# Kernel optimization log

Measured on AMD Instinct MI355X. Metric: run time of the kernel, lower is better.

Reference implementation:

```python
import jax, jax.numpy as jnp
import numpy as np

B, I, J, K, F = 16, 2048, 1024, 1024, 32

def _xavier(key, shape):
    fan_in, fan_out = shape[0], shape[1]
    limit = np.sqrt(6.0 / (fan_in + fan_out))
    return jax.random.uniform(key, shape, jnp.float32, -limit, limit)

def setup_inputs() -> dict:
    key = jax.random.key(0)
    kx, kwx, kwy, kwz = jax.random.split(key, 4)
    return {
        "matrix_batch": jax.random.normal(kx, (B, I, J), jnp.float32),
        "W_x": _xavier(kwx, (I, F)),
        "W_y": _xavier(kwy, (J, F)),
        "W_z": _xavier(kwz, (K, F)),
    }

def reference(matrix_batch, W_x, W_y, W_z):
    # Original math: W[i,j,k] = sum_f Wx[i,f]*Wy[j,f]*Wz[k,f];
    #                out[b,i,k] = sum_j x[b,i,j] * W[i,j,k]
    # Fused two-stage contraction (never materializes the (I,J,K) core):
    # t[b,i,f] = (sum_j x[b,i,j] Wy[j,f]) * Wx[i,f]
    t = jnp.einsum('bij,jf->bif', matrix_batch, W_y) * W_x[None, :, :]
    out = jnp.einsum('bif,kf->bik', t, W_z)  # (B, I, K)
    return out
```

## Files before the change

### kernel.cpp

```cpp
#include <hip/hip_runtime.h>
#include <hip/hip_bf16.h>
#include <string.h>

constexpr int kI = 2048;
constexpr int kJ = 1024;
constexpr int kK = 1024;
constexpr int kF = 32;
constexpr int kRows = 16 * 2048;

typedef __attribute__((ext_vector_type(8))) short short8v;
typedef __attribute__((ext_vector_type(4))) float f32x4;

__device__ inline unsigned short bf16_hi_bits(float v) {
    __hip_bfloat16 h = __float2bfloat16(v);
    unsigned short s;
    memcpy(&s, &h, 2);
    return s;
}
__device__ inline float bf16_bits_to_f(unsigned short s) {
    unsigned u = (unsigned)s << 16;
    float f;
    memcpy(&f, &u, 4);
    return f;
}
__device__ inline short8v as_s8(uint4 u) {
    union { uint4 a; short8v b; } c;
    c.a = u;
    return c.b;
}
__device__ inline void gl_lds16(const void* g, void* l) {
    __builtin_amdgcn_global_load_lds(
        (const __attribute__((address_space(1))) void*)g,
        (__attribute__((address_space(3))) void*)l,
        16, 0, 0);
}

__global__ __launch_bounds__(128)
void ge_prepack(const float* __restrict__ Wy, uint4* __restrict__ wyp)
{
    const int e  = blockIdx.x * 128 + threadIdx.x;
    const int l  = e & 63;
    const int h  = (e >> 6) & 1;
    const int tf = (e >> 7) & 1;
    const int ks = e >> 8;
    const int f  = (l & 15) + tf * 16;
    const int j0 = ks * 32 + (l >> 4) * 8;

    unsigned d[4];
#pragma unroll
    for (int p = 0; p < 4; ++p) {
        const float v0 = Wy[(size_t)(j0 + 2 * p) * kF + f];
        const float v1 = Wy[(size_t)(j0 + 2 * p + 1) * kF + f];
        unsigned short s0, s1;
        if (h == 0) {
            s0 = bf16_hi_bits(v0);
            s1 = bf16_hi_bits(v1);
        } else {
            s0 = bf16_hi_bits(v0 - bf16_bits_to_f(bf16_hi_bits(v0)));
            s1 = bf16_hi_bits(v1 - bf16_bits_to_f(bf16_hi_bits(v1)));
        }
        d[p] = (unsigned)s0 | ((unsigned)s1 << 16);
    }
    wyp[e] = make_uint4(d[0], d[1], d[2], d[3]);
}

__global__ __launch_bounds__(128)
void ge_prepack_z(const float* __restrict__ Wz, uint4* __restrict__ wzp)
{
    const int e  = blockIdx.x * 128 + threadIdx.x;
    const int l  = e & 63;
    const int h  = (e >> 6) & 1;
    const int nt = e >> 7;
    const int n  = nt * 16 + (l & 15);
    const int f0 = (l >> 4) * 8;

    unsigned d[4];
#pragma unroll
    for (int p = 0; p < 4; ++p) {
        const float v0 = Wz[(size_t)n * kF + f0 + 2 * p];
        const float v1 = Wz[(size_t)n * kF + f0 + 2 * p + 1];
        unsigned short s0, s1;
        if (h == 0) {
            s0 = bf16_hi_bits(v0);
            s1 = bf16_hi_bits(v1);
        } else {
            s0 = bf16_hi_bits(v0 - bf16_bits_to_f(bf16_hi_bits(v0)));
            s1 = bf16_hi_bits(v1 - bf16_bits_to_f(bf16_hi_bits(v1)));
        }
        d[p] = (unsigned)s0 | ((unsigned)s1 << 16);
    }
    wzp[e] = make_uint4(d[0], d[1], d[2], d[3]);
}

__global__ __launch_bounds__(256, 2)
void ge_fused_mfma(const float* __restrict__ x,
                   const float* __restrict__ Wx,
                   const uint4* __restrict__ wyp,
                   const uint4* __restrict__ wzp,
                   float* __restrict__ out)
{
    __shared__ __align__(16) char smem[73728];
    float4* xb4 = reinterpret_cast<float4*>(smem);
    uint4*  bb4 = reinterpret_cast<uint4*>(smem + 49152);
    uint4*  zb  = reinterpret_cast<uint4*>(smem);
    float*  t2  = reinterpret_cast<float*>(smem + 49152);

    const int tid  = threadIdx.x;
    const int lane = tid & 63;
    const int wv   = tid >> 6;
    const int mrow = lane & 15;
    const int g    = lane >> 4;
    const int rowBase = blockIdx.x * 64;

    f32x4 c0 = {0.f, 0.f, 0.f, 0.f};
    f32x4 c1 = {0.f, 0.f, 0.f, 0.f};

#define STAGE(buf, ti)                                                  \
    {                                                                   \
        _Pragma("unroll")                                               \
        for (int q = 0; q < 4; ++q) {                                   \
            const int srow = wv * 16 + q * 4 + (lane >> 4);             \
            const int sc   = lane & 15;                                 \
            gl_lds16(x + (size_t)(rowBase + srow) * kJ + (ti) * 64      \
                       + 4 * (sc ^ (srow & 7)),                         \
                     &xb4[(buf) * 1024 + (wv * 16 + q * 4) * 16]);      \
        }                                                               \
        _Pragma("unroll")                                               \
        for (int q = 0; q < 2; ++q)                                     \
            gl_lds16(wyp + (size_t)(ti) * 512 + wv * 128 + q * 64 + lane, \
                     &bb4[(buf) * 512 + wv * 128 + q * 64]);            \
    }

    STAGE(0, 0)

#pragma unroll
    for (int ti = 0; ti < 16; ++ti) {
        const int bufR = ti % 3;
        if (ti < 15) {
            STAGE((ti + 1) % 3, ti + 1)
            asm volatile("s_waitcnt vmcnt(6) lgkmcnt(0)" ::: "memory");
        } else {
            asm volatile("s_waitcnt vmcnt(0) lgkmcnt(0)" ::: "memory");
        }
        asm volatile("s_barrier" ::: "memory");
        __builtin_amdgcn_sched_barrier(0);

#pragma unroll
        for (int kk2 = 0; kk2 < 2; ++kk2) {
            const uint4 b0h = bb4[bufR * 512 + kk2 * 256 + lane];
            const uint4 b0l = bb4[bufR * 512 + kk2 * 256 + 64 + lane];
            const uint4 b1h = bb4[bufR * 512 + kk2 * 256 + 128 + lane];
            const uint4 b1l = bb4[bufR * 512 + kk2 * 256 + 192 + lane];

            const int s0 = (kk2 * 8 + g * 2) ^ (mrow & 7);
            const int s1 = (kk2 * 8 + g * 2 + 1) ^ (mrow & 7);
            const float4 xa = xb4[bufR * 1024 + (wv * 16 + mrow) * 16 + s0];
            const float4 xc = xb4[bufR * 1024 + (wv * 16 + mrow) * 16 + s1];
            const float xv[8] = {xa.x, xa.y, xa.z, xa.w,
                                 xc.x, xc.y, xc.z, xc.w};

            short8v ah, al;
#pragma unroll
            for (int e = 0; e < 8; ++e) {
                const unsigned short hb = bf16_hi_bits(xv[e]);
                const float hf = bf16_bits_to_f(hb);
                const unsigned short lb = bf16_hi_bits(xv[e] - hf);
                ah[e] = (short)hb;
                al[e] = (short)lb;
            }

            c0 = __builtin_amdgcn_mfma_f32_16x16x32_bf16(ah, as_s8(b0h), c0, 0, 0, 0);
            c1 = __builtin_amdgcn_mfma_f32_16x16x32_bf16(ah, as_s8(b1h), c1, 0, 0, 0);
            c0 = __builtin_amdgcn_mfma_f32_16x16x32_bf16(ah, as_s8(b0l), c0, 0, 0, 0);
            c1 = __builtin_amdgcn_mfma_f32_16x16x32_bf16(ah, as_s8(b1l), c1, 0, 0, 0);
            c0 = __builtin_amdgcn_mfma_f32_16x16x32_bf16(al, as_s8(b0h), c0, 0, 0, 0);
            c1 = __builtin_amdgcn_mfma_f32_16x16x32_bf16(al, as_s8(b1h), c1, 0, 0, 0);
        }
    }
#undef STAGE

    __syncthreads();
    {
        const int n = lane & 15;
#pragma unroll
        for (int r = 0; r < 4; ++r) {
            const int rl = wv * 16 + g * 4 + r;
            const int i  = (rowBase + rl) & (kI - 1);
            t2[rl * 36 + n]      = c0[r] * Wx[(size_t)i * kF + n];
            t2[rl * 36 + 16 + n] = c1[r] * Wx[(size_t)i * kF + 16 + n];
        }
    }
    __syncthreads();

    short8v th, tl;
    {
        const float* trow = &t2[(wv * 16 + mrow) * 36 + g * 8];
        const float4 ta = *reinterpret_cast<const float4*>(trow);
        const float4 tb = *reinterpret_cast<const float4*>(trow + 4);
        const float tv[8] = {ta.x, ta.y, ta.z, ta.w, tb.x, tb.y, tb.z, tb.w};
#pragma unroll
        for (int e = 0; e < 8; ++e) {
            const unsigned short hb = bf16_hi_bits(tv[e]);
            const float hf = bf16_bits_to_f(hb);
            const unsigned short lb = bf16_hi_bits(tv[e] - hf);
            th[e] = (short)hb;
            tl[e] = (short)lb;
        }
    }

    const int n = lane & 15;
#pragma unroll
    for (int ch = 0; ch < 4; ++ch) {
        __syncthreads();
#pragma unroll
        for (int q = 0; q < 8; ++q)
            gl_lds16(wzp + (size_t)ch * 2048 + wv * 512 + q * 64 + lane,
                     &zb[wv * 512 + q * 64]);
        asm volatile("s_waitcnt vmcnt(0)" ::: "memory");
        __syncthreads();

#pragma unroll
        for (int ntl = 0; ntl < 16; ++ntl) {
            const uint4 bh = zb[ntl * 128 + lane];
            const uint4 bl = zb[ntl * 128 + 64 + lane];

            f32x4 c = {0.f, 0.f, 0.f, 0.f};
            c = __builtin_amdgcn_mfma_f32_16x16x32_bf16(th, as_s8(bh), c, 0, 0, 0);
            c = __builtin_amdgcn_mfma_f32_16x16x32_bf16(th, as_s8(bl), c, 0, 0, 0);
            c = __builtin_amdgcn_mfma_f32_16x16x32_bf16(tl, as_s8(bh), c, 0, 0, 0);

            const int k = ch * 256 + ntl * 16 + n;
#pragma unroll
            for (int r = 0; r < 4; ++r) {
                const int row = rowBase + wv * 16 + g * 4 + r;
                out[(size_t)row * kK + k] = c[r];
            }
        }
    }
}

__global__ __launch_bounds__(256, 2)
void gated_encoder_fused(const float* __restrict__ x,
                         const float* __restrict__ Wx,
                         const float* __restrict__ Wy,
                         const float* __restrict__ Wz,
                         float* __restrict__ out)
{
    __shared__ float t2[64][kF + 4];

    const int tid  = threadIdx.x;
    const int lane = tid & 63;
    const int wv   = tid >> 6;

    const int rloc = wv * 16 + (lane >> 2);
    const int row  = blockIdx.x * 64 + rloc;
    const int fg8  = (lane & 3) * 8;

    const float* __restrict__ xrow = x + (size_t)row * kJ;

    float acc[8];
#pragma unroll
    for (int u = 0; u < 8; ++u) acc[u] = 0.0f;

    for (int j = 0; j < kJ; j += 8) {
        const float4 xv0 = *reinterpret_cast<const float4*>(xrow + j);
        const float4 xv1 = *reinterpret_cast<const float4*>(xrow + j + 4);
        const float xs[8] = {xv0.x, xv0.y, xv0.z, xv0.w,
                             xv1.x, xv1.y, xv1.z, xv1.w};
#pragma unroll
        for (int u = 0; u < 8; ++u) {
            const float* wyp = Wy + (size_t)(j + u) * kF + fg8;
            const float4 w0 = *reinterpret_cast<const float4*>(wyp);
            const float4 w1 = *reinterpret_cast<const float4*>(wyp + 4);
            acc[0] = fmaf(xs[u], w0.x, acc[0]);
            acc[1] = fmaf(xs[u], w0.y, acc[1]);
            acc[2] = fmaf(xs[u], w0.z, acc[2]);
            acc[3] = fmaf(xs[u], w0.w, acc[3]);
            acc[4] = fmaf(xs[u], w1.x, acc[4]);
            acc[5] = fmaf(xs[u], w1.y, acc[5]);
            acc[6] = fmaf(xs[u], w1.z, acc[6]);
            acc[7] = fmaf(xs[u], w1.w, acc[7]);
        }
    }

    const int i = row & (kI - 1);
    const float* wxp = Wx + (size_t)i * kF + fg8;
    const float4 g0 = *reinterpret_cast<const float4*>(wxp);
    const float4 g1 = *reinterpret_cast<const float4*>(wxp + 4);
    float4 r0, r1;
    r0.x = acc[0] * g0.x;  r0.y = acc[1] * g0.y;
    r0.z = acc[2] * g0.z;  r0.w = acc[3] * g0.w;
    r1.x = acc[4] * g1.x;  r1.y = acc[5] * g1.y;
    r1.z = acc[6] * g1.z;  r1.w = acc[7] * g1.w;
    *reinterpret_cast<float4*>(&t2[rloc][fg8])     = r0;
    *reinterpret_cast<float4*>(&t2[rloc][fg8 + 4]) = r1;

    __syncthreads();

    const size_t outBase = (size_t)blockIdx.x * 64 * kK;

#pragma unroll
    for (int pass = 0; pass < 2; ++pass) {
        const int k1 = pass * 512 + tid;
        const int k2 = k1 + 256;
        const float* wz1 = Wz + (size_t)k1 * kF;
        const float* wz2 = Wz + (size_t)k2 * kF;
        float4 z1[8], z2[8];
#pragma unroll
        for (int m = 0; m < 8; ++m) {
            z1[m] = *reinterpret_cast<const float4*>(wz1 + 4 * m);
            z2[m] = *reinterpret_cast<const float4*>(wz2 + 4 * m);
        }
        for (int r = 0; r < 64; ++r) {
            float4 a1 = {0.f, 0.f, 0.f, 0.f};
            float4 a2 = {0.f, 0.f, 0.f, 0.f};
#pragma unroll
            for (int m = 0; m < 8; ++m) {
                const float4 tv = *reinterpret_cast<const float4*>(&t2[r][4 * m]);
                a1.x = fmaf(tv.x, z1[m].x, a1.x);
                a1.y = fmaf(tv.y, z1[m].y, a1.y);
                a1.z = fmaf(tv.z, z1[m].z, a1.z);
                a1.w = fmaf(tv.w, z1[m].w, a1.w);
                a2.x = fmaf(tv.x, z2[m].x, a2.x);
                a2.y = fmaf(tv.y, z2[m].y, a2.y);
                a2.z = fmaf(tv.z, z2[m].z, a2.z);
                a2.w = fmaf(tv.w, z2[m].w, a2.w);
            }
            out[outBase + (size_t)r * kK + k1] = (a1.x + a1.y) + (a1.z + a1.w);
            out[outBase + (size_t)r * kK + k2] = (a2.x + a2.y) + (a2.z + a2.w);
        }
    }
}

extern "C" void kernel_launch(void* const* d_in, const int* in_sizes, int n_in,
                              void* d_out, int out_size, void* d_ws, size_t ws_size,
                              hipStream_t stream) {
    const float* x  = (const float*)d_in[0];
    const float* Wx = (const float*)d_in[1];
    const float* Wy = (const float*)d_in[2];
    const float* Wz = (const float*)d_in[3];
    float* out = (float*)d_out;

    const size_t wyBytes = 8192 * sizeof(uint4);
    const size_t wzBytes = 8192 * sizeof(uint4);

    if (ws_size >= wyBytes + wzBytes && d_ws != nullptr) {
        uint4* wyp = (uint4*)d_ws;
        uint4* wzp = (uint4*)((char*)d_ws + wyBytes);
        ge_prepack<<<dim3(64), 128, 0, stream>>>(Wy, wyp);
        ge_prepack_z<<<dim3(64), 128, 0, stream>>>(Wz, wzp);
        ge_fused_mfma<<<dim3(kRows / 64), 256, 0, stream>>>(x, Wx, wyp, wzp, out);
    } else {
        gated_encoder_fused<<<dim3(kRows / 64), 256, 0, stream>>>(x, Wx, Wy, Wz, out);
    }
}
```

Measured before the change: 53.90 us.

## Deepen x/Wy prefetch to two stages, double-buffer Wz, merge prepack kernels

The main loop now keeps two tiles in flight. It issues the x/Wy load for tile ti+2 after the barrier instead of ti+1 before it, so a single barrier guards the triple buffer. The Wz phase gets a double-buffered LDS region whose next chunk is prefetched while the current chunk's MFMAs and output stores run, replacing the serial load-wait-sync pattern. The t2 scratch moves to offset 64 KiB, and LDS grows slightly to 75776 bytes. The two prepack kernels are merged into one launch to cut launch overhead, with occupancy risk from the larger shared-memory footprint.

```diff
diff --git a/kernel.cpp b/kernel.cpp
--- a/kernel.cpp
+++ b/kernel.cpp
@@ -36,60 +36,58 @@
 }
 
 __global__ __launch_bounds__(128)
-void ge_prepack(const float* __restrict__ Wy, uint4* __restrict__ wyp)
+void ge_prepack_all(const float* __restrict__ Wy, const float* __restrict__ Wz,
+                    uint4* __restrict__ wyp, uint4* __restrict__ wzp)
 {
-    const int e  = blockIdx.x * 128 + threadIdx.x;
-    const int l  = e & 63;
-    const int h  = (e >> 6) & 1;
-    const int tf = (e >> 7) & 1;
-    const int ks = e >> 8;
-    const int f  = (l & 15) + tf * 16;
-    const int j0 = ks * 32 + (l >> 4) * 8;
-
-    unsigned d[4];
-#pragma unroll
-    for (int p = 0; p < 4; ++p) {
-        const float v0 = Wy[(size_t)(j0 + 2 * p) * kF + f];
-        const float v1 = Wy[(size_t)(j0 + 2 * p + 1) * kF + f];
-        unsigned short s0, s1;
-        if (h == 0) {
-            s0 = bf16_hi_bits(v0);
-            s1 = bf16_hi_bits(v1);
-        } else {
-            s0 = bf16_hi_bits(v0 - bf16_bits_to_f(bf16_hi_bits(v0)));
-            s1 = bf16_hi_bits(v1 - bf16_bits_to_f(bf16_hi_bits(v1)));
-        }
-        d[p] = (unsigned)s0 | ((unsigned)s1 << 16);
-    }
-    wyp[e] = make_uint4(d[0], d[1], d[2], d[3]);
-}
-
-__global__ __launch_bounds__(128)
-void ge_prepack_z(const float* __restrict__ Wz, uint4* __restrict__ wzp)
-{
-    const int e  = blockIdx.x * 128 + threadIdx.x;
-    const int l  = e & 63;
-    const int h  = (e >> 6) & 1;
-    const int nt = e >> 7;
-    const int n  = nt * 16 + (l & 15);
-    const int f0 = (l >> 4) * 8;
-
-    unsigned d[4];
-#pragma unroll
-    for (int p = 0; p < 4; ++p) {
-        const float v0 = Wz[(size_t)n * kF + f0 + 2 * p];
-        const float v1 = Wz[(size_t)n * kF + f0 + 2 * p + 1];
-        unsigned short s0, s1;
-        if (h == 0) {
-            s0 = bf16_hi_bits(v0);
-            s1 = bf16_hi_bits(v1);
-        } else {
-            s0 = bf16_hi_bits(v0 - bf16_bits_to_f(bf16_hi_bits(v0)));
-            s1 = bf16_hi_bits(v1 - bf16_bits_to_f(bf16_hi_bits(v1)));
-        }
-        d[p] = (unsigned)s0 | ((unsigned)s1 << 16);
-    }
-    wzp[e] = make_uint4(d[0], d[1], d[2], d[3]);
+    const int eg = blockIdx.x * 128 + threadIdx.x;
+    if (eg < 8192) {
+        const int e  = eg;
+        const int l  = e & 63;
+        const int h  = (e >> 6) & 1;
+        const int tf = (e >> 7) & 1;
+        const int ks = e >> 8;
+        const int f  = (l & 15) + tf * 16;
+        const int j0 = ks * 32 + (l >> 4) * 8;
+        unsigned d[4];
+#pragma unroll
+        for (int p = 0; p < 4; ++p) {
+            const float v0 = Wy[(size_t)(j0 + 2 * p) * kF + f];
+            const float v1 = Wy[(size_t)(j0 + 2 * p + 1) * kF + f];
+            unsigned short s0, s1;
+            if (h == 0) {
+                s0 = bf16_hi_bits(v0);
+                s1 = bf16_hi_bits(v1);
+            } else {
+                s0 = bf16_hi_bits(v0 - bf16_bits_to_f(bf16_hi_bits(v0)));
+                s1 = bf16_hi_bits(v1 - bf16_bits_to_f(bf16_hi_bits(v1)));
+            }
+            d[p] = (unsigned)s0 | ((unsigned)s1 << 16);
+        }
+        wyp[e] = make_uint4(d[0], d[1], d[2], d[3]);
+    } else {
+        const int e  = eg - 8192;
+        const int l  = e & 63;
+        const int h  = (e >> 6) & 1;
+        const int nt = e >> 7;
+        const int n  = nt * 16 + (l & 15);
+        const int f0 = (l >> 4) * 8;
+        unsigned d[4];
+#pragma unroll
+        for (int p = 0; p < 4; ++p) {
+            const float v0 = Wz[(size_t)n * kF + f0 + 2 * p];
+            const float v1 = Wz[(size_t)n * kF + f0 + 2 * p + 1];
+            unsigned short s0, s1;
+            if (h == 0) {
+                s0 = bf16_hi_bits(v0);
+                s1 = bf16_hi_bits(v1);
+            } else {
+                s0 = bf16_hi_bits(v0 - bf16_bits_to_f(bf16_hi_bits(v0)));
+                s1 = bf16_hi_bits(v1 - bf16_bits_to_f(bf16_hi_bits(v1)));
+            }
+            d[p] = (unsigned)s0 | ((unsigned)s1 << 16);
+        }
+        wzp[e] = make_uint4(d[0], d[1], d[2], d[3]);
+    }
 }
 
 __global__ __launch_bounds__(256, 2)
@@ -99,11 +97,11 @@
                    const uint4* __restrict__ wzp,
                    float* __restrict__ out)
 {
-    __shared__ __align__(16) char smem[73728];
+    __shared__ __align__(16) char smem[75776];
     float4* xb4 = reinterpret_cast<float4*>(smem);
     uint4*  bb4 = reinterpret_cast<uint4*>(smem + 49152);
     uint4*  zb  = reinterpret_cast<uint4*>(smem);
-    float*  t2  = reinterpret_cast<float*>(smem + 49152);
+    float*  t2  = reinterpret_cast<float*>(smem + 65536);
 
     const int tid  = threadIdx.x;
     const int lane = tid & 63;
@@ -132,18 +130,19 @@
     }
 
     STAGE(0, 0)
+    STAGE(1, 1)
 
 #pragma unroll
     for (int ti = 0; ti < 16; ++ti) {
         const int bufR = ti % 3;
         if (ti < 15) {
-            STAGE((ti + 1) % 3, ti + 1)
             asm volatile("s_waitcnt vmcnt(6) lgkmcnt(0)" ::: "memory");
         } else {
             asm volatile("s_waitcnt vmcnt(0) lgkmcnt(0)" ::: "memory");
         }
         asm volatile("s_barrier" ::: "memory");
         __builtin_amdgcn_sched_barrier(0);
+        if (ti < 14) { STAGE((ti + 2) % 3, ti + 2) }
 
 #pragma unroll
         for (int kk2 = 0; kk2 < 2; ++kk2) {
@@ -192,6 +191,14 @@
     }
     __syncthreads();
 
+#define STAGE_Z(buf, ch)                                                \
+    _Pragma("unroll")                                                   \
+    for (int q = 0; q < 8; ++q)                                         \
+        gl_lds16(wzp + (size_t)(ch) * 2048 + wv * 512 + q * 64 + lane,  \
+                 &zb[(buf) * 2048 + wv * 512 + q * 64]);
+
+    STAGE_Z(0, 0)
+
     short8v th, tl;
     {
         const float* trow = &t2[(wv * 16 + mrow) * 36 + g * 8];
@@ -211,18 +218,19 @@
     const int n = lane & 15;
 #pragma unroll
     for (int ch = 0; ch < 4; ++ch) {
-        __syncthreads();
-#pragma unroll
-        for (int q = 0; q < 8; ++q)
-            gl_lds16(wzp + (size_t)ch * 2048 + wv * 512 + q * 64 + lane,
-                     &zb[wv * 512 + q * 64]);
-        asm volatile("s_waitcnt vmcnt(0)" ::: "memory");
-        __syncthreads();
+        if (ch < 3) {
+            asm volatile("s_waitcnt vmcnt(8) lgkmcnt(0)" ::: "memory");
+        } else {
+            asm volatile("s_waitcnt vmcnt(0) lgkmcnt(0)" ::: "memory");
+        }
+        asm volatile("s_barrier" ::: "memory");
+        __builtin_amdgcn_sched_barrier(0);
+        if (ch < 3) { STAGE_Z((ch + 1) & 1, ch + 1) }
 
 #pragma unroll
         for (int ntl = 0; ntl < 16; ++ntl) {
-            const uint4 bh = zb[ntl * 128 + lane];
-            const uint4 bl = zb[ntl * 128 + 64 + lane];
+            const uint4 bh = zb[(ch & 1) * 2048 + ntl * 128 + lane];
+            const uint4 bl = zb[(ch & 1) * 2048 + ntl * 128 + 64 + lane];
 
             f32x4 c = {0.f, 0.f, 0.f, 0.f};
             c = __builtin_amdgcn_mfma_f32_16x16x32_bf16(th, as_s8(bh), c, 0, 0, 0);
@@ -237,6 +245,7 @@
             }
         }
     }
+#undef STAGE_Z
 }
 
 __global__ __launch_bounds__(256, 2)
@@ -347,8 +356,7 @@
     if (ws_size >= wyBytes + wzBytes && d_ws != nullptr) {
         uint4* wyp = (uint4*)d_ws;
         uint4* wzp = (uint4*)((char*)d_ws + wyBytes);
-        ge_prepack<<<dim3(64), 128, 0, stream>>>(Wy, wyp);
-        ge_prepack_z<<<dim3(64), 128, 0, stream>>>(Wz, wzp);
+        ge_prepack_all<<<dim3(128), 128, 0, stream>>>(Wy, Wz, wyp, wzp);
         ge_fused_mfma<<<dim3(kRows / 64), 256, 0, stream>>>(x, Wx, wyp, wzp, out);
     } else {
         gated_encoder_fused<<<dim3(kRows / 64), 256, 0, stream>>>(x, Wx, Wy, Wz, out);
```

Result: faster. 51.95 us (median of 2 runs) (-3.6%).
